# Kernel tuning notes

Measured on AMD Instinct MI355X. Metric: run time of the kernel, lower is better.

Reference implementation:

```python
import jax, jax.numpy as jnp
import numpy as np

N_EXPERTS = 64
TOP_K = 8
NORM_TOPK = True
SCALING = 1.0


def setup_inputs() -> dict:
    key = jax.random.key(0)
    logits = jax.random.normal(key, (524288, N_EXPERTS), dtype=jnp.float32)
    return {"logits": logits}


def reference(logits):
    # scoring_func == 'softmax': softmax over expert dim in float32
    routing_weights = jax.nn.softmax(logits.astype(jnp.float32), axis=1)
    # top-k experts per token: values and indices, sorted descending (matches torch.topk)
    topk_weights, topk_ids = jax.lax.top_k(routing_weights, TOP_K)  # [T, K]
    if NORM_TOPK:
        topk_weights = topk_weights / jnp.sum(topk_weights, axis=-1, keepdims=True)
    if SCALING != 1.0:
        topk_weights = topk_weights * SCALING
    # torch.histc(topk_ids, bins=E, min=0, max=E) == bincount over flat ids (float output)
    tokens_per_expert = jnp.zeros((N_EXPERTS,), dtype=jnp.float32).at[topk_ids.ravel()].add(1.0)
    return (logits, routing_weights, topk_weights, topk_ids, tokens_per_expert)
```

## Files before the change

kernel.cpp:

```cpp
#include <hip/hip_runtime.h>
#include <math.h>

#define NEXP 64
#define TOPK 8
#define TILE 128
#define HPITCH 33

typedef float v4 __attribute__((ext_vector_type(4)));

__global__ __launch_bounds__(TILE, 4) void router_kernel(
    const float* __restrict__ logits,
    float* __restrict__ out_logits,
    float* __restrict__ out_rw,
    float* __restrict__ out_tw,
    float* __restrict__ out_ti,
    float* __restrict__ out_hist,
    int nTiles)
{
    __shared__ float halfbuf[2][64 * HPITCH];
    __shared__ float shist[NEXP];

    const int tid = threadIdx.x;
    const int w   = tid >> 6;
    const int l   = tid & 63;
    const int q   = l & 15;
    if (tid < NEXP) shist[tid] = 0.0f;
    __syncthreads();

    float* __restrict__ hb = &halfbuf[w][0];

    #pragma unroll
    for (int t = 0; t < 2; ++t) {
        const int tb = blockIdx.x + t * gridDim.x;
        if (tb >= nTiles) break;
        const long waveBase = (long)tb * TILE + (w << 6);

        const v4* g = (const v4*)logits + waveBase * (NEXP / 4);
        v4 row[16];
        #pragma unroll
        for (int k = 0; k < 16; ++k)
            row[k] = __builtin_nontemporal_load(&g[l + (k << 6)]);

        v4* gp = (v4*)out_logits + waveBase * (NEXP / 4);
        #pragma unroll
        for (int k = 0; k < 16; ++k)
            gp[l + (k << 6)] = row[k];

        if (q < 8) {
            #pragma unroll
            for (int k = 0; k < 16; ++k) {
                int r = (l >> 4) + (k << 2);
                float* b = &hb[r * HPITCH + (q << 2)];
                v4 v = row[k];
                b[0] = v.x; b[1] = v.y; b[2] = v.z; b[3] = v.w;
            }
        }

        const float* __restrict__ myrow = &hb[l * HPITCH];
        float vals[TOPK], ids[TOPK];
        #pragma unroll
        for (int j = 0; j < TOPK; ++j) { vals[j] = -INFINITY; ids[j] = 0.0f; }
        float ssum = 0.0f;

        #pragma unroll 8
        for (int e = 0; e < 32; ++e) {
            float x = myrow[e];
            ssum += __expf(x);
            float fe = (float)e;
            bool c[TOPK];
            #pragma unroll
            for (int j = 0; j < TOPK; ++j) c[j] = x > vals[j];
            #pragma unroll
            for (int j = TOPK - 1; j >= 1; --j) {
                ids[j]  = c[j] ? (c[j - 1] ? ids[j - 1] : fe) : ids[j];
                vals[j] = __builtin_amdgcn_fmed3f(x, vals[j - 1], vals[j]);
            }
            ids[0]  = c[0] ? fe : ids[0];
            vals[0] = fmaxf(vals[0], x);
        }

        if (q >= 8) {
            #pragma unroll
            for (int k = 0; k < 16; ++k) {
                int r = (l >> 4) + (k << 2);
                float* b = &hb[r * HPITCH + ((q - 8) << 2)];
                v4 v = row[k];
                b[0] = v.x; b[1] = v.y; b[2] = v.z; b[3] = v.w;
            }
        }

        #pragma unroll 8
        for (int e = 32; e < NEXP; ++e) {
            float x = myrow[e - 32];
            ssum += __expf(x);
            float fe = (float)e;
            bool c[TOPK];
            #pragma unroll
            for (int j = 0; j < TOPK; ++j) c[j] = x > vals[j];
            #pragma unroll
            for (int j = TOPK - 1; j >= 1; --j) {
                ids[j]  = c[j] ? (c[j - 1] ? ids[j - 1] : fe) : ids[j];
                vals[j] = __builtin_amdgcn_fmed3f(x, vals[j - 1], vals[j]);
            }
            ids[0]  = c[0] ? fe : ids[0];
            vals[0] = fmaxf(vals[0], x);
        }
        const float sinv = 1.0f / ssum;

        float ew[TOPK];
        float tsum = 0.0f;
        #pragma unroll
        for (int j = 0; j < TOPK; ++j) { ew[j] = __expf(vals[j]); tsum += ew[j]; }
        const float tinv = 1.0f / tsum;

        const long tok = waveBase + l;
        v4* twp = (v4*)out_tw + tok * 2;
        v4* tip = (v4*)out_ti + tok * 2;
        v4 w0 = { ew[0] * tinv, ew[1] * tinv, ew[2] * tinv, ew[3] * tinv };
        v4 w1 = { ew[4] * tinv, ew[5] * tinv, ew[6] * tinv, ew[7] * tinv };
        v4 i0 = { ids[0], ids[1], ids[2], ids[3] };
        v4 i1 = { ids[4], ids[5], ids[6], ids[7] };
        twp[0] = w0;
        twp[1] = w1;
        tip[0] = i0;
        tip[1] = i1;

        #pragma unroll
        for (int j = 0; j < TOPK; ++j)
            atomicAdd(&shist[(int)ids[j]], 1.0f);

        v4* grw = (v4*)out_rw + waveBase * (NEXP / 4);
        #pragma unroll
        for (int k = 0; k < 16; ++k) {
            float si = __shfl(sinv, (l >> 4) + (k << 2));
            v4 x = row[k];
            v4 o;
            o.x = __expf(x.x) * si;
            o.y = __expf(x.y) * si;
            o.z = __expf(x.z) * si;
            o.w = __expf(x.w) * si;
            grw[l + (k << 6)] = o;
        }
    }

    __syncthreads();
    if (tid < NEXP) atomicAdd(&out_hist[tid], shist[tid]);
}

extern "C" void kernel_launch(void* const* d_in, const int* in_sizes, int n_in,
                              void* d_out, int out_size, void* d_ws, size_t ws_size,
                              hipStream_t stream) {
    const float* logits = (const float*)d_in[0];
    const long T = (long)in_sizes[0] / NEXP;

    float* out      = (float*)d_out;
    float* o_logits = out;
    float* o_rw     = out + T * NEXP;
    float* o_tw     = out + 2 * T * NEXP;
    float* o_ti     = o_tw + T * TOPK;
    float* o_hist   = o_ti + T * TOPK;

    (void)hipMemsetAsync(o_hist, 0, NEXP * sizeof(float), stream);

    const int nTiles = (int)(T / TILE);
    const int grid   = (nTiles + 1) / 2;
    router_kernel<<<grid, TILE, 0, stream>>>(logits, o_logits, o_rw, o_tw, o_ti,
                                             o_hist, nTiles);
}
```

Measured before the change: 104.6 us.

## Split router into top-k kernel and streaming softmax/copy kernel

Replaces the single fused kernel with two passes when workspace is available. The first pass computes per-token top-k, softmax normalizer and histogram with one thread per row, storing the inverse sum to workspace. The second pass is a grid-stride stream that copies logits and writes the softmax weights. It removes the LDS transpose and register pressure of the fused kernel, but re-reads the logits from memory, adding traffic to a bandwidth-bound workload.

```diff
diff --git a/kernel.cpp b/kernel.cpp
--- a/kernel.cpp
+++ b/kernel.cpp
@@ -3,12 +3,94 @@
 
 #define NEXP 64
 #define TOPK 8
+
+typedef float v4 __attribute__((ext_vector_type(4)));
+
+__global__ __launch_bounds__(256) void topk_kernel(
+    const float* __restrict__ logits,
+    float* __restrict__ out_tw,
+    float* __restrict__ out_ti,
+    float* __restrict__ out_hist,
+    float* __restrict__ sinv_ws)
+{
+    __shared__ float shist[NEXP];
+    const int tid = threadIdx.x;
+    if (tid < NEXP) shist[tid] = 0.0f;
+    __syncthreads();
+
+    const long tok = (long)blockIdx.x * 256 + tid;
+    const v4* g = (const v4*)logits + tok * (NEXP / 4);
+
+    float vals[TOPK], ids[TOPK];
+    #pragma unroll
+    for (int j = 0; j < TOPK; ++j) { vals[j] = -INFINITY; ids[j] = 0.0f; }
+    float ssum = 0.0f;
+
+    #pragma unroll
+    for (int k = 0; k < 16; ++k) {
+        v4 x4 = __builtin_nontemporal_load(&g[k]);
+        #pragma unroll
+        for (int u = 0; u < 4; ++u) {
+            float x = x4[u];
+            ssum += __expf(x);
+            float fe = (float)(k * 4 + u);
+            bool c[TOPK];
+            #pragma unroll
+            for (int j = 0; j < TOPK; ++j) c[j] = x > vals[j];
+            #pragma unroll
+            for (int j = TOPK - 1; j >= 1; --j) {
+                ids[j]  = c[j] ? (c[j - 1] ? ids[j - 1] : fe) : ids[j];
+                vals[j] = __builtin_amdgcn_fmed3f(x, vals[j - 1], vals[j]);
+            }
+            ids[0]  = c[0] ? fe : ids[0];
+            vals[0] = fmaxf(vals[0], x);
+        }
+    }
+    sinv_ws[tok] = 1.0f / ssum;
+
+    float ew[TOPK];
+    float tsum = 0.0f;
+    #pragma unroll
+    for (int j = 0; j < TOPK; ++j) { ew[j] = __expf(vals[j]); tsum += ew[j]; }
+    const float tinv = 1.0f / tsum;
+
+    v4* twp = (v4*)out_tw + tok * 2;
+    v4* tip = (v4*)out_ti + tok * 2;
+    v4 w0 = { ew[0] * tinv, ew[1] * tinv, ew[2] * tinv, ew[3] * tinv };
+    v4 w1 = { ew[4] * tinv, ew[5] * tinv, ew[6] * tinv, ew[7] * tinv };
+    v4 i0 = { ids[0], ids[1], ids[2], ids[3] };
+    v4 i1 = { ids[4], ids[5], ids[6], ids[7] };
+    twp[0] = w0; twp[1] = w1;
+    tip[0] = i0; tip[1] = i1;
+
+    #pragma unroll
+    for (int j = 0; j < TOPK; ++j)
+        atomicAdd(&shist[(int)ids[j]], 1.0f);
+    __syncthreads();
+    if (tid < NEXP) atomicAdd(&out_hist[tid], shist[tid]);
+}
+
+__global__ __launch_bounds__(256) void stream_kernel(
+    const float* __restrict__ logits,
+    const float* __restrict__ sinv_ws,
+    float* __restrict__ out_logits,
+    float* __restrict__ out_rw,
+    long n4)
+{
+    const long stride = (long)gridDim.x * 256;
+    for (long i = (long)blockIdx.x * 256 + threadIdx.x; i < n4; i += stride) {
+        v4 x = ((const v4*)logits)[i];
+        float si = sinv_ws[i >> 4];
+        ((v4*)out_logits)[i] = x;
+        v4 o = { __expf(x.x) * si, __expf(x.y) * si,
+                 __expf(x.z) * si, __expf(x.w) * si };
+        ((v4*)out_rw)[i] = o;
+    }
+}
+
 #define TILE 128
 #define HPITCH 33
-
-typedef float v4 __attribute__((ext_vector_type(4)));
-
-__global__ __launch_bounds__(TILE, 4) void router_kernel(
+__global__ __launch_bounds__(TILE, 4) void router_mono(
     const float* __restrict__ logits,
     float* __restrict__ out_logits,
     float* __restrict__ out_rw,
@@ -19,14 +101,10 @@
 {
     __shared__ float halfbuf[2][64 * HPITCH];
     __shared__ float shist[NEXP];
-
     const int tid = threadIdx.x;
-    const int w   = tid >> 6;
-    const int l   = tid & 63;
-    const int q   = l & 15;
+    const int w = tid >> 6, l = tid & 63, q = l & 15;
     if (tid < NEXP) shist[tid] = 0.0f;
     __syncthreads();
-
     float* __restrict__ hb = &halfbuf[w][0];
 
     #pragma unroll
@@ -34,18 +112,14 @@
         const int tb = blockIdx.x + t * gridDim.x;
         if (tb >= nTiles) break;
         const long waveBase = (long)tb * TILE + (w << 6);
-
         const v4* g = (const v4*)logits + waveBase * (NEXP / 4);
         v4 row[16];
         #pragma unroll
         for (int k = 0; k < 16; ++k)
             row[k] = __builtin_nontemporal_load(&g[l + (k << 6)]);
-
         v4* gp = (v4*)out_logits + waveBase * (NEXP / 4);
         #pragma unroll
-        for (int k = 0; k < 16; ++k)
-            gp[l + (k << 6)] = row[k];
-
+        for (int k = 0; k < 16; ++k) gp[l + (k << 6)] = row[k];
         if (q < 8) {
             #pragma unroll
             for (int k = 0; k < 16; ++k) {
@@ -55,13 +129,11 @@
                 b[0] = v.x; b[1] = v.y; b[2] = v.z; b[3] = v.w;
             }
         }
-
         const float* __restrict__ myrow = &hb[l * HPITCH];
         float vals[TOPK], ids[TOPK];
         #pragma unroll
         for (int j = 0; j < TOPK; ++j) { vals[j] = -INFINITY; ids[j] = 0.0f; }
         float ssum = 0.0f;
-
         #pragma unroll 8
         for (int e = 0; e < 32; ++e) {
             float x = myrow[e];
@@ -78,7 +150,6 @@
             ids[0]  = c[0] ? fe : ids[0];
             vals[0] = fmaxf(vals[0], x);
         }
-
         if (q >= 8) {
             #pragma unroll
             for (int k = 0; k < 16; ++k) {
@@ -88,7 +159,6 @@
                 b[0] = v.x; b[1] = v.y; b[2] = v.z; b[3] = v.w;
             }
         }
-
         #pragma unroll 8
         for (int e = 32; e < NEXP; ++e) {
             float x = myrow[e - 32];
@@ -106,13 +176,11 @@
             vals[0] = fmaxf(vals[0], x);
         }
         const float sinv = 1.0f / ssum;
-
         float ew[TOPK];
         float tsum = 0.0f;
         #pragma unroll
         for (int j = 0; j < TOPK; ++j) { ew[j] = __expf(vals[j]); tsum += ew[j]; }
         const float tinv = 1.0f / tsum;
-
         const long tok = waveBase + l;
         v4* twp = (v4*)out_tw + tok * 2;
         v4* tip = (v4*)out_ti + tok * 2;
@@ -120,29 +188,20 @@
         v4 w1 = { ew[4] * tinv, ew[5] * tinv, ew[6] * tinv, ew[7] * tinv };
         v4 i0 = { ids[0], ids[1], ids[2], ids[3] };
         v4 i1 = { ids[4], ids[5], ids[6], ids[7] };
-        twp[0] = w0;
-        twp[1] = w1;
-        tip[0] = i0;
-        tip[1] = i1;
-
+        twp[0] = w0; twp[1] = w1; tip[0] = i0; tip[1] = i1;
         #pragma unroll
         for (int j = 0; j < TOPK; ++j)
             atomicAdd(&shist[(int)ids[j]], 1.0f);
-
         v4* grw = (v4*)out_rw + waveBase * (NEXP / 4);
         #pragma unroll
         for (int k = 0; k < 16; ++k) {
             float si = __shfl(sinv, (l >> 4) + (k << 2));
             v4 x = row[k];
-            v4 o;
-            o.x = __expf(x.x) * si;
-            o.y = __expf(x.y) * si;
-            o.z = __expf(x.z) * si;
-            o.w = __expf(x.w) * si;
+            v4 o = { __expf(x.x) * si, __expf(x.y) * si,
+                     __expf(x.z) * si, __expf(x.w) * si };
             grw[l + (k << 6)] = o;
         }
     }
-
     __syncthreads();
     if (tid < NEXP) atomicAdd(&out_hist[tid], shist[tid]);
 }
@@ -162,8 +221,16 @@
 
     (void)hipMemsetAsync(o_hist, 0, NEXP * sizeof(float), stream);
 
-    const int nTiles = (int)(T / TILE);
-    const int grid   = (nTiles + 1) / 2;
-    router_kernel<<<grid, TILE, 0, stream>>>(logits, o_logits, o_rw, o_tw, o_ti,
-                                             o_hist, nTiles);
-}
+    if (ws_size >= (size_t)T * sizeof(float)) {
+        float* sinv_ws = (float*)d_ws;
+        const int grid1 = (int)(T / 256);
+        topk_kernel<<<grid1, 256, 0, stream>>>(logits, o_tw, o_ti, o_hist, sinv_ws);
+        const long n4 = T * (NEXP / 4);
+        stream_kernel<<<2048, 256, 0, stream>>>(logits, sinv_ws, o_logits, o_rw, n4);
+    } else {
+        const int nTiles = (int)(T / TILE);
+        const int grid   = (nTiles + 1) / 2;
+        router_mono<<<grid, TILE, 0, stream>>>(logits, o_logits, o_rw, o_tw, o_ti,
+                                               o_hist, nTiles);
+    }
+}
```

After: 188.5 us. +80.3%, slower.
